# Optimization experiments

Measured on AMD Instinct MI355X. Metric: run time of the kernel, lower is better.

Reference implementation:

```python
import jax, jax.numpy as jnp
import numpy as np

NUM_IN = 1024
HIDDEN = 32  # pooling_hidden_dim fixed in PoolingFunction
N = 200000


def setup_inputs() -> dict:
    key = jax.random.key(0)
    ks = jax.random.split(key, 7)
    s_in = 1.0 / np.sqrt(NUM_IN)
    s_h = 1.0 / np.sqrt(HIDDEN)
    return {
        "x": jax.random.normal(ks[0], (N, NUM_IN), dtype=jnp.float32),
        "V_w": jax.random.uniform(ks[1], (HIDDEN, NUM_IN), jnp.float32, -s_in, s_in),
        "V_b": jax.random.uniform(ks[2], (HIDDEN,), jnp.float32, -s_in, s_in),
        "U_w": jax.random.uniform(ks[3], (HIDDEN, NUM_IN), jnp.float32, -s_in, s_in),
        "U_b": jax.random.uniform(ks[4], (HIDDEN,), jnp.float32, -s_in, s_in),
        "w_w": jax.random.uniform(ks[5], (1, HIDDEN), jnp.float32, -s_h, s_h),
        "w_b": jax.random.uniform(ks[6], (1,), jnp.float32, -s_h, s_h),
    }


def reference(x, V_w, V_b, U_w, U_b, w_w, w_b):
    # x: [N, num_in]
    a_v = jnp.tanh(x @ V_w.T + V_b)          # [N, H]
    a_u = jax.nn.sigmoid(x @ U_w.T + U_b)    # [N, H]
    a = (a_v * a_u) @ w_w.T + w_b            # [N, 1] attention logits
    a = jax.nn.softmax(a.T, axis=1)          # [1, N]
    m = a @ x                                # [1, num_in]
    return m
```

## Files before the change

kernel.cpp:

```cpp
#include <hip/hip_runtime.h>
#include <math.h>

#define NUM_IN 1024
#define TILE_R 16
#define NB_MAX 256
#define PR_OSTRIDE 17
#define PR_QSTRIDE (64 * PR_OSTRIDE + 4)

using bf16x8 = __attribute__((ext_vector_type(8))) short;
using f32x4  = __attribute__((ext_vector_type(4))) float;

__device__ __forceinline__ unsigned int f2bf1(float f) {
  unsigned int u = __float_as_uint(f);
  return (u + 0x7fffu + ((u >> 16) & 1u)) >> 16;
}
__device__ __forceinline__ unsigned int pk2(float a, float b) {
  return f2bf1(a) | (f2bf1(b) << 16);
}
__device__ __forceinline__ float bflo(unsigned int w) { return __uint_as_float(w << 16); }
__device__ __forceinline__ float bfhi(unsigned int w) { return __uint_as_float(w & 0xffff0000u); }

#define BARX() do { \
  __builtin_amdgcn_sched_barrier(0); \
  asm volatile("s_waitcnt lgkmcnt(0)" ::: "memory"); \
  __builtin_amdgcn_s_barrier(); \
  __builtin_amdgcn_sched_barrier(0); \
} while (0)

#define WAIT_VM(n) do { \
  __builtin_amdgcn_sched_barrier(0); \
  asm volatile("s_waitcnt vmcnt(" #n ")" ::: "memory"); \
  __builtin_amdgcn_sched_barrier(0); \
} while (0)

__global__ __launch_bounds__(512, 1) void ga_main(
    const float* __restrict__ x,
    const float* __restrict__ Vw, const float* __restrict__ Uw,
    const float* __restrict__ Vb, const float* __restrict__ Ub,
    const float* __restrict__ ww, const float* __restrict__ wb,
    float* __restrict__ wsAcc, float* __restrict__ wsM, float* __restrict__ wsS,
    int nb, int nTiles)
{
  __shared__ __align__(16) float prered[8 * PR_QSTRIDE];
  __shared__ __align__(16) float lgs[TILE_R];

  const int tid = threadIdx.x;
  const int b   = blockIdx.x;
  const int w   = tid >> 6;
  const int l   = tid & 63;
  const int l15 = l & 15;
  const int kg  = l >> 4;
  const int h   = tid & 31;
  const int rr  = tid >> 5;

  const float vbh = Vb[h], ubh = Ub[h], wwh = ww[h];
  const float wb0 = wb[0];

  uint4 bfr[4][4];
  {
    #pragma unroll
    for (int nt = 0; nt < 4; ++nt) {
      const int o = (nt << 4) + l15;
      const float* Wr = (o < 32) ? (Vw + (size_t)o * NUM_IN) : (Uw + (size_t)(o - 32) * NUM_IN);
      #pragma unroll
      for (int s = 0; s < 4; ++s) {
        const int k0 = (w << 7) + (s << 5) + (kg << 3);
        const float4 a = *reinterpret_cast<const float4*>(Wr + k0);
        const float4 c = *reinterpret_cast<const float4*>(Wr + k0 + 4);
        uint4 v;
        v.x = pk2(a.x, a.y); v.y = pk2(a.z, a.w);
        v.z = pk2(c.x, c.y); v.w = pk2(c.z, c.w);
        bfr[nt][s] = v;
      }
    }
    #pragma unroll
    for (int nt = 0; nt < 4; ++nt)
      #pragma unroll
      for (int s = 0; s < 4; ++s)
        asm volatile("" : "+v"(bfr[nt][s].x), "+v"(bfr[nt][s].y),
                          "+v"(bfr[nt][s].z), "+v"(bfr[nt][s].w));
  }

  const char* xb8 = (const char*)x;
  const int inRow = (w << 9) + (kg << 5);

  float4 sA0[4], sB0[4], sA1[4], sB1[4];
  uint4  xf[4];

  #define ISSUE_SET(sa, sb, Tt) do { \
    __builtin_amdgcn_sched_barrier(0); \
    const int Tc_ = ((Tt) < nTiles) ? (Tt) : (nTiles - 1); \
    const char* base_ = xb8 + ((size_t)Tc_ * TILE_R + l15) * 4096 + inRow; \
    sa[0] = *reinterpret_cast<const float4*>(base_      );  sb[0] = *reinterpret_cast<const float4*>(base_ +  16); \
    sa[1] = *reinterpret_cast<const float4*>(base_ + 128);  sb[1] = *reinterpret_cast<const float4*>(base_ + 144); \
    sa[2] = *reinterpret_cast<const float4*>(base_ + 256);  sb[2] = *reinterpret_cast<const float4*>(base_ + 272); \
    sa[3] = *reinterpret_cast<const float4*>(base_ + 384);  sb[3] = *reinterpret_cast<const float4*>(base_ + 400); \
    __builtin_amdgcn_sched_barrier(0); \
  } while (0)

  #define PACK_SET(sa, sb) do { \
    _Pragma("unroll") \
    for (int s = 0; s < 4; ++s) { \
      xf[s].x = pk2(sa[s].x, sa[s].y); xf[s].y = pk2(sa[s].z, sa[s].w); \
      xf[s].z = pk2(sb[s].x, sb[s].y); xf[s].w = pk2(sb[s].z, sb[s].w); \
    } \
    _Pragma("unroll") \
    for (int s = 0; s < 4; ++s) \
      asm volatile("" : "+v"(xf[s].x), "+v"(xf[s].y), "+v"(xf[s].z), "+v"(xf[s].w)); \
  } while (0)

  float M = -INFINITY, S = 0.f;
  float acc[4][8];
  #pragma unroll
  for (int s = 0; s < 4; ++s)
    #pragma unroll
    for (int i = 0; i < 8; ++i) acc[s][i] = 0.f;

  int T = b;

  #define COMPUTE_TILE() do { \
    { \
      f32x4 a4[4] = {{0.f,0.f,0.f,0.f},{0.f,0.f,0.f,0.f},{0.f,0.f,0.f,0.f},{0.f,0.f,0.f,0.f}}; \
      _Pragma("unroll") \
      for (int s = 0; s < 4; ++s) { \
        const bf16x8 af = __builtin_bit_cast(bf16x8, xf[s]); \
        _Pragma("unroll") \
        for (int nt = 0; nt < 4; ++nt) \
          a4[nt] = __builtin_amdgcn_mfma_f32_16x16x32_bf16( \
              af, __builtin_bit_cast(bf16x8, bfr[nt][s]), a4[nt], 0, 0, 0); \
      } \
      _Pragma("unroll") \
      for (int nt = 0; nt < 4; ++nt) { \
        const int obase = w * PR_QSTRIDE + ((nt << 4) + l15) * PR_OSTRIDE + (kg << 2); \
        _Pragma("unroll") \
        for (int r = 0; r < 4; ++r) prered[obase + r] = a4[nt][r]; \
      } \
    } \
    BARX(); \
    { \
      float pv = vbh, pu = ubh; \
      _Pragma("unroll") \
      for (int q = 0; q < 8; ++q) { \
        pv += prered[q * PR_QSTRIDE + h * PR_OSTRIDE + rr]; \
        pu += prered[q * PR_QSTRIDE + (h + 32) * PR_OSTRIDE + rr]; \
      } \
      const float ev = __expf(2.f * pv); \
      const float av = (ev - 1.f) * __builtin_amdgcn_rcpf(ev + 1.f); \
      const float au = __builtin_amdgcn_rcpf(1.f + __expf(-pu)); \
      float g = av * au * wwh; \
      g += __shfl_xor(g, 1); \
      g += __shfl_xor(g, 2); \
      g += __shfl_xor(g, 4); \
      g += __shfl_xor(g, 8); \
      g += __shfl_xor(g, 16); \
      if (h == 0) lgs[rr] = g + wb0; \
    } \
    BARX(); \
    { \
      const float lf = lgs[l15]; \
      float mc = lf; \
      mc = fmaxf(mc, __shfl_xor(mc, 1)); \
      mc = fmaxf(mc, __shfl_xor(mc, 2)); \
      mc = fmaxf(mc, __shfl_xor(mc, 4)); \
      mc = fmaxf(mc, __shfl_xor(mc, 8)); \
      if (mc > M) { \
        const float scale = __expf(M - mc); \
        S *= scale; \
        _Pragma("unroll") \
        for (int s = 0; s < 4; ++s) \
          _Pragma("unroll") \
          for (int i = 0; i < 8; ++i) acc[s][i] *= scale; \
        M = mc; \
      } \
      const float p = __expf(lf - M); \
      S += p; \
      _Pragma("unroll") \
      for (int s = 0; s < 4; ++s) { \
        acc[s][0] = fmaf(p, bflo(xf[s].x), acc[s][0]); \
        acc[s][1] = fmaf(p, bfhi(xf[s].x), acc[s][1]); \
        acc[s][2] = fmaf(p, bflo(xf[s].y), acc[s][2]); \
        acc[s][3] = fmaf(p, bfhi(xf[s].y), acc[s][3]); \
        acc[s][4] = fmaf(p, bflo(xf[s].z), acc[s][4]); \
        acc[s][5] = fmaf(p, bfhi(xf[s].z), acc[s][5]); \
        acc[s][6] = fmaf(p, bflo(xf[s].w), acc[s][6]); \
        acc[s][7] = fmaf(p, bfhi(xf[s].w), acc[s][7]); \
      } \
    } \
  } while (0)

  ISSUE_SET(sA0, sB0, T);
  WAIT_VM(0);
  PACK_SET(sA0, sB0);
  ISSUE_SET(sA0, sB0, T + nb);
  ISSUE_SET(sA1, sB1, T + 2 * nb);

  while (true) {
    COMPUTE_TILE();
    if ((T + nb) >= nTiles) break;
    WAIT_VM(8);
    PACK_SET(sA0, sB0);
    ISSUE_SET(sA0, sB0, T + 3 * nb);
    T += nb;

    COMPUTE_TILE();
    if ((T + nb) >= nTiles) break;
    WAIT_VM(8);
    PACK_SET(sA1, sB1);
    ISSUE_SET(sA1, sB1, T + 3 * nb);
    T += nb;
  }

  #pragma unroll
  for (int d = 1; d < 16; d <<= 1) {
    #pragma unroll
    for (int s = 0; s < 4; ++s)
      #pragma unroll
      for (int i = 0; i < 8; ++i) acc[s][i] += __shfl_xor(acc[s][i], d);
    S += __shfl_xor(S, d);
  }
  if (l15 == 0) {
    #pragma unroll
    for (int s = 0; s < 4; ++s) {
      float* dst = &wsAcc[(size_t)b * NUM_IN + (w << 7) + (s << 5) + (kg << 3)];
      *reinterpret_cast<float4*>(dst)     = make_float4(acc[s][0], acc[s][1], acc[s][2], acc[s][3]);
      *reinterpret_cast<float4*>(dst + 4) = make_float4(acc[s][4], acc[s][5], acc[s][6], acc[s][7]);
    }
  }
  if (tid == 0) { wsM[b] = M; wsS[b] = S; }
}

__global__ void ga_reduceMS(const float* __restrict__ wsM, const float* __restrict__ wsS,
                            float* __restrict__ wsW, float* __restrict__ wsT, int nb)
{
  __shared__ float sm[8], ss[8];
  const int t = threadIdx.x;
  float m = (t < nb) ? wsM[t] : -INFINITY;
  float mm = m;
  #pragma unroll
  for (int d = 1; d < 64; d <<= 1) mm = fmaxf(mm, __shfl_xor(mm, d));
  if ((t & 63) == 0) sm[t >> 6] = mm;
  __syncthreads();
  const float M = fmaxf(fmaxf(fmaxf(sm[0], sm[1]), fmaxf(sm[2], sm[3])),
                        fmaxf(fmaxf(sm[4], sm[5]), fmaxf(sm[6], sm[7])));
  const float wg = (t < nb) ? __expf(m - M) : 0.f;
  if (t < nb) wsW[t] = wg;
  float s = wg * ((t < nb) ? wsS[t] : 0.f);
  #pragma unroll
  for (int d = 1; d < 64; d <<= 1) s += __shfl_xor(s, d);
  if ((t & 63) == 0) ss[t >> 6] = s;
  __syncthreads();
  if (t == 0) {
    float St = 0.f;
    #pragma unroll
    for (int k = 0; k < 8; ++k) St += ss[k];
    wsT[0] = St;
  }
}

__global__ void ga_combine(const float* __restrict__ wsAcc, const float* __restrict__ wsW,
                           const float* __restrict__ wsT, float* __restrict__ out, int nb)
{
  __shared__ float red[8][32];
  const int t = threadIdx.x;
  const int col = (blockIdx.x << 5) + (t & 31);
  const int seg = t >> 5;
  float s = 0.f;
  for (int ii = 0; ii < 64; ++ii) {
    const int i = (seg << 6) + ii;
    if (i < nb) s = fmaf(wsW[i], wsAcc[(size_t)i * NUM_IN + col], s);
  }
  red[seg][t & 31] = s;
  __syncthreads();
  if (seg == 0) {
    float tot = 0.f;
    #pragma unroll
    for (int k = 0; k < 8; ++k) tot += red[k][t];
    out[col] = tot / wsT[0];
  }
}

extern "C" void kernel_launch(void* const* d_in, const int* in_sizes, int n_in,
                              void* d_out, int out_size, void* d_ws, size_t ws_size,
                              hipStream_t stream)
{
  const float* x  = (const float*)d_in[0];
  const float* Vw = (const float*)d_in[1];
  const float* Vb = (const float*)d_in[2];
  const float* Uw = (const float*)d_in[3];
  const float* Ub = (const float*)d_in[4];
  const float* ww = (const float*)d_in[5];
  const float* wb = (const float*)d_in[6];
  float* out = (float*)d_out;

  const int Nrows  = in_sizes[0] / NUM_IN;
  const int nTiles = Nrows / TILE_R;

  const size_t per = (size_t)NUM_IN * 4 + 16;
  int nb = (int)((ws_size - 64) / per);
  if (nb > NB_MAX)  nb = NB_MAX;
  if (nb > nTiles)  nb = nTiles;
  if (nb < 1)       nb = 1;

  float* wsAcc = (float*)d_ws;
  float* wsM   = wsAcc + (size_t)nb * NUM_IN;
  float* wsS   = wsM + nb;
  float* wsW   = wsS + nb;
  float* wsT   = wsW + nb;

  ga_main<<<nb, 512, 0, stream>>>(x, Vw, Uw, Vb, Ub, ww, wb, wsAcc, wsM, wsS, nb, nTiles);
  ga_reduceMS<<<1, 512, 0, stream>>>(wsM, wsS, wsW, wsT, nb);
  ga_combine<<<32, 256, 0, stream>>>(wsAcc, wsW, wsT, out, nb);
}
```

Before: 178.6 us.

## Software-pipeline tile phases to remove one barrier per tile, swizzle LDS layout

Splits the per-tile work into MFMA, activation and accumulate phases, double-buffers the LDS partial sums, logits and packed x registers, and skews the accumulate of the previous tile after the activation of the current one. This cuts the barriers per tile from two to one. It also replaces the padded LDS layout with an XOR-swizzled [row][output] layout to avoid bank conflicts. In exchange it doubles LDS use and adds one more set of packed x registers, which raises register pressure.

```diff
diff --git a/kernel.cpp b/kernel.cpp
--- a/kernel.cpp
+++ b/kernel.cpp
@@ -4,8 +4,6 @@
 #define NUM_IN 1024
 #define TILE_R 16
 #define NB_MAX 256
-#define PR_OSTRIDE 17
-#define PR_QSTRIDE (64 * PR_OSTRIDE + 4)
 
 using bf16x8 = __attribute__((ext_vector_type(8))) short;
 using f32x4  = __attribute__((ext_vector_type(4))) float;
@@ -41,8 +39,8 @@
     float* __restrict__ wsAcc, float* __restrict__ wsM, float* __restrict__ wsS,
     int nb, int nTiles)
 {
-  __shared__ __align__(16) float prered[8 * PR_QSTRIDE];
-  __shared__ __align__(16) float lgs[TILE_R];
+  __shared__ __align__(16) float prered[2][8][16][64];
+  __shared__ __align__(16) float lgs[2][16];
 
   const int tid = threadIdx.x;
   const int b   = blockIdx.x;
@@ -52,6 +50,8 @@
   const int kg  = l >> 4;
   const int h   = tid & 31;
   const int rr  = tid >> 5;
+  const int xsw = (kg & 1) << 4;
+  const int xsr = ((rr >> 2) & 1) << 4;
 
   const float vbh = Vb[h], ubh = Ub[h], wwh = ww[h];
   const float wb0 = wb[0];
@@ -85,7 +85,7 @@
   const int inRow = (w << 9) + (kg << 5);
 
   float4 sA0[4], sB0[4], sA1[4], sB1[4];
-  uint4  xf[4];
+  uint4  xfA[4], xfB[4];
 
   #define ISSUE_SET(sa, sb, Tt) do { \
     __builtin_amdgcn_sched_barrier(0); \
@@ -98,15 +98,15 @@
     __builtin_amdgcn_sched_barrier(0); \
   } while (0)
 
-  #define PACK_SET(sa, sb) do { \
+  #define PACK_SET(dst, sa, sb) do { \
     _Pragma("unroll") \
     for (int s = 0; s < 4; ++s) { \
-      xf[s].x = pk2(sa[s].x, sa[s].y); xf[s].y = pk2(sa[s].z, sa[s].w); \
-      xf[s].z = pk2(sb[s].x, sb[s].y); xf[s].w = pk2(sb[s].z, sb[s].w); \
+      dst[s].x = pk2(sa[s].x, sa[s].y); dst[s].y = pk2(sa[s].z, sa[s].w); \
+      dst[s].z = pk2(sb[s].x, sb[s].y); dst[s].w = pk2(sb[s].z, sb[s].w); \
     } \
     _Pragma("unroll") \
     for (int s = 0; s < 4; ++s) \
-      asm volatile("" : "+v"(xf[s].x), "+v"(xf[s].y), "+v"(xf[s].z), "+v"(xf[s].w)); \
+      asm volatile("" : "+v"(dst[s].x), "+v"(dst[s].y), "+v"(dst[s].z), "+v"(dst[s].w)); \
   } while (0)
 
   float M = -INFINITY, S = 0.f;
@@ -116,99 +116,112 @@
     #pragma unroll
     for (int i = 0; i < 8; ++i) acc[s][i] = 0.f;
 
-  int T = b;
-
-  #define COMPUTE_TILE() do { \
-    { \
-      f32x4 a4[4] = {{0.f,0.f,0.f,0.f},{0.f,0.f,0.f,0.f},{0.f,0.f,0.f,0.f},{0.f,0.f,0.f,0.f}}; \
+  #define MFMA_PHASE(xfS, pb) do { \
+    f32x4 a4[4] = {{0.f,0.f,0.f,0.f},{0.f,0.f,0.f,0.f},{0.f,0.f,0.f,0.f},{0.f,0.f,0.f,0.f}}; \
+    _Pragma("unroll") \
+    for (int s = 0; s < 4; ++s) { \
+      const bf16x8 af = __builtin_bit_cast(bf16x8, xfS[s]); \
       _Pragma("unroll") \
-      for (int s = 0; s < 4; ++s) { \
-        const bf16x8 af = __builtin_bit_cast(bf16x8, xf[s]); \
+      for (int nt = 0; nt < 4; ++nt) \
+        a4[nt] = __builtin_amdgcn_mfma_f32_16x16x32_bf16( \
+            af, __builtin_bit_cast(bf16x8, bfr[nt][s]), a4[nt], 0, 0, 0); \
+    } \
+    _Pragma("unroll") \
+    for (int nt = 0; nt < 4; ++nt) \
+      _Pragma("unroll") \
+      for (int r = 0; r < 4; ++r) \
+        prered[pb][w][(kg << 2) + r][((nt << 4) + l15) ^ xsw] = a4[nt][r]; \
+  } while (0)
+
+  #define ACT_PHASE(pb, lb) do { \
+    float pv = vbh, pu = ubh; \
+    _Pragma("unroll") \
+    for (int q = 0; q < 8; ++q) { \
+      pv += prered[pb][q][rr][h ^ xsr]; \
+      pu += prered[pb][q][rr][(h + 32) ^ xsr]; \
+    } \
+    const float ev = __expf(2.f * pv); \
+    const float av = (ev - 1.f) * __builtin_amdgcn_rcpf(ev + 1.f); \
+    const float au = __builtin_amdgcn_rcpf(1.f + __expf(-pu)); \
+    float g = av * au * wwh; \
+    g += __shfl_xor(g, 1); \
+    g += __shfl_xor(g, 2); \
+    g += __shfl_xor(g, 4); \
+    g += __shfl_xor(g, 8); \
+    g += __shfl_xor(g, 16); \
+    if (h == 0) lgs[lb][rr] = g + wb0; \
+  } while (0)
+
+  #define ACC_PHASE(xfS, lb) do { \
+    const float lf = lgs[lb][l15]; \
+    float mc = lf; \
+    mc = fmaxf(mc, __shfl_xor(mc, 1)); \
+    mc = fmaxf(mc, __shfl_xor(mc, 2)); \
+    mc = fmaxf(mc, __shfl_xor(mc, 4)); \
+    mc = fmaxf(mc, __shfl_xor(mc, 8)); \
+    if (mc > M) { \
+      const float scale = __expf(M - mc); \
+      S *= scale; \
+      _Pragma("unroll") \
+      for (int s = 0; s < 4; ++s) \
         _Pragma("unroll") \
-        for (int nt = 0; nt < 4; ++nt) \
-          a4[nt] = __builtin_amdgcn_mfma_f32_16x16x32_bf16( \
-              af, __builtin_bit_cast(bf16x8, bfr[nt][s]), a4[nt], 0, 0, 0); \
-      } \
-      _Pragma("unroll") \
-      for (int nt = 0; nt < 4; ++nt) { \
-        const int obase = w * PR_QSTRIDE + ((nt << 4) + l15) * PR_OSTRIDE + (kg << 2); \
-        _Pragma("unroll") \
-        for (int r = 0; r < 4; ++r) prered[obase + r] = a4[nt][r]; \
-      } \
-    } \
-    BARX(); \
-    { \
-      float pv = vbh, pu = ubh; \
-      _Pragma("unroll") \
-      for (int q = 0; q < 8; ++q) { \
-        pv += prered[q * PR_QSTRIDE + h * PR_OSTRIDE + rr]; \
-        pu += prered[q * PR_QSTRIDE + (h + 32) * PR_OSTRIDE + rr]; \
-      } \
-      const float ev = __expf(2.f * pv); \
-      const float av = (ev - 1.f) * __builtin_amdgcn_rcpf(ev + 1.f); \
-      const float au = __builtin_amdgcn_rcpf(1.f + __expf(-pu)); \
-      float g = av * au * wwh; \
-      g += __shfl_xor(g, 1); \
-      g += __shfl_xor(g, 2); \
-      g += __shfl_xor(g, 4); \
-      g += __shfl_xor(g, 8); \
-      g += __shfl_xor(g, 16); \
-      if (h == 0) lgs[rr] = g + wb0; \
-    } \
-    BARX(); \
-    { \
-      const float lf = lgs[l15]; \
-      float mc = lf; \
-      mc = fmaxf(mc, __shfl_xor(mc, 1)); \
-      mc = fmaxf(mc, __shfl_xor(mc, 2)); \
-      mc = fmaxf(mc, __shfl_xor(mc, 4)); \
-      mc = fmaxf(mc, __shfl_xor(mc, 8)); \
-      if (mc > M) { \
-        const float scale = __expf(M - mc); \
-        S *= scale; \
-        _Pragma("unroll") \
-        for (int s = 0; s < 4; ++s) \
-          _Pragma("unroll") \
-          for (int i = 0; i < 8; ++i) acc[s][i] *= scale; \
-        M = mc; \
-      } \
-      const float p = __expf(lf - M); \
-      S += p; \
-      _Pragma("unroll") \
-      for (int s = 0; s < 4; ++s) { \
-        acc[s][0] = fmaf(p, bflo(xf[s].x), acc[s][0]); \
-        acc[s][1] = fmaf(p, bfhi(xf[s].x), acc[s][1]); \
-        acc[s][2] = fmaf(p, bflo(xf[s].y), acc[s][2]); \
-        acc[s][3] = fmaf(p, bfhi(xf[s].y), acc[s][3]); \
-        acc[s][4] = fmaf(p, bflo(xf[s].z), acc[s][4]); \
-        acc[s][5] = fmaf(p, bfhi(xf[s].z), acc[s][5]); \
-        acc[s][6] = fmaf(p, bflo(xf[s].w), acc[s][6]); \
-        acc[s][7] = fmaf(p, bfhi(xf[s].w), acc[s][7]); \
-      } \
-    } \
-  } while (0)
-
-  ISSUE_SET(sA0, sB0, T);
+        for (int i = 0; i < 8; ++i) acc[s][i] *= scale; \
+      M = mc; \
+    } \
+    const float p = __expf(lf - M); \
+    S += p; \
+    _Pragma("unroll") \
+    for (int s = 0; s < 4; ++s) { \
+      acc[s][0] = fmaf(p, bflo(xfS[s].x), acc[s][0]); \
+      acc[s][1] = fmaf(p, bfhi(xfS[s].x), acc[s][1]); \
+      acc[s][2] = fmaf(p, bflo(xfS[s].y), acc[s][2]); \
+      acc[s][3] = fmaf(p, bfhi(xfS[s].y), acc[s][3]); \
+      acc[s][4] = fmaf(p, bflo(xfS[s].z), acc[s][4]); \
+      acc[s][5] = fmaf(p, bfhi(xfS[s].z), acc[s][5]); \
+      acc[s][6] = fmaf(p, bflo(xfS[s].w), acc[s][6]); \
+      acc[s][7] = fmaf(p, bfhi(xfS[s].w), acc[s][7]); \
+    } \
+  } while (0)
+
+  ISSUE_SET(sA0, sB0, b);
   WAIT_VM(0);
-  PACK_SET(sA0, sB0);
-  ISSUE_SET(sA0, sB0, T + nb);
-  ISSUE_SET(sA1, sB1, T + 2 * nb);
-
-  while (true) {
-    COMPUTE_TILE();
-    if ((T + nb) >= nTiles) break;
-    WAIT_VM(8);
-    PACK_SET(sA0, sB0);
-    ISSUE_SET(sA0, sB0, T + 3 * nb);
-    T += nb;
-
-    COMPUTE_TILE();
-    if ((T + nb) >= nTiles) break;
-    WAIT_VM(8);
-    PACK_SET(sA1, sB1);
-    ISSUE_SET(sA1, sB1, T + 3 * nb);
-    T += nb;
-  }
+  PACK_SET(xfA, sA0, sB0);
+  ISSUE_SET(sA0, sB0, b + nb);
+  ISSUE_SET(sA1, sB1, b + 2 * nb);
+  MFMA_PHASE(xfA, 0);
+  BARX();
+  ACT_PHASE(0, 0);
+  WAIT_VM(8);
+  PACK_SET(xfB, sA0, sB0);
+  ISSUE_SET(sA0, sB0, b + 3 * nb);
+
+  int Tk = b + nb;
+  int lastPar = 0;
+  if (Tk < nTiles) {
+    while (true) {
+      MFMA_PHASE(xfB, 1);
+      BARX();
+      ACT_PHASE(1, 1);
+      ACC_PHASE(xfA, 0);
+      WAIT_VM(8);
+      PACK_SET(xfA, sA1, sB1);
+      ISSUE_SET(sA1, sB1, Tk + 3 * nb);
+      Tk += nb;
+      if (Tk >= nTiles) { lastPar = 1; break; }
+
+      MFMA_PHASE(xfA, 0);
+      BARX();
+      ACT_PHASE(0, 0);
+      ACC_PHASE(xfB, 1);
+      WAIT_VM(8);
+      PACK_SET(xfB, sA0, sB0);
+      ISSUE_SET(sA0, sB0, Tk + 3 * nb);
+      Tk += nb;
+      if (Tk >= nTiles) { lastPar = 0; break; }
+    }
+  }
+  BARX();
+  if (lastPar) { ACC_PHASE(xfB, 1); } else { ACC_PHASE(xfA, 0); }
 
   #pragma unroll
   for (int d = 1; d < 16; d <<= 1) {
```

After: 174.5 us. -2.3%, faster.
